# Performance work log

Hardware: AMD Instinct MI355X
Metric: run time of the kernel (lower is better)

## Reference

```python
import jax, jax.numpy as jnp
import numpy as np

N = 8192
X_DIM = 256
Y_DIM = 256


def setup_inputs() -> dict:
    key = jax.random.key(0)
    kx, ky, kw = jax.random.split(key, 3)
    x_samples = jax.random.normal(kx, (N, X_DIM), dtype=jnp.float32)
    y_samples = jax.random.normal(ky, (N, Y_DIM), dtype=jnp.float32)
    # kaiming-uniform-ish init for the bilinear weight [x_dim, y_dim]
    bound = float(np.sqrt(6.0 / X_DIM))
    w = jax.random.uniform(kw, (X_DIM, Y_DIM), dtype=jnp.float32,
                           minval=-bound, maxval=bound)
    return {"x_samples": x_samples, "y_samples": y_samples, "w": w}


def reference(x_samples, y_samples, w):
    # Pairwise bilinear scores S[i, b] = x[i] @ W @ y[b]
    # (equivalent to the original's tiled einsum, without O(N^2*dim) tiles)
    n = y_samples.shape[0]
    xw = x_samples @ w                      # [N, y_dim]
    S = xw @ y_samples.T                    # [N, N], S[i, b]
    # T0[i] = S[i, i]; T1.logsumexp(dim=1)[b] = logsumexp_i S[i, b]
    t0_mean = jnp.mean(jnp.diagonal(S))
    lse_mean = jnp.mean(jax.nn.logsumexp(S, axis=0))
    lower_bound = t0_mean - (lse_mean - jnp.log(jnp.float32(n)))
    return lower_bound
```

## Files before the change

### kernel.cpp

```cpp
#include <hip/hip_runtime.h>

typedef __attribute__((ext_vector_type(8))) short bf16x8;
typedef __attribute__((ext_vector_type(4))) float f32x4;
typedef __attribute__((ext_vector_type(8))) int   i32x8;
typedef __attribute__((ext_vector_type(4))) int   i32x4;

union OpU { i32x8 v; i32x4 h[2]; };

__device__ __forceinline__ unsigned short f2bf(float f) {
    unsigned int u = __float_as_uint(f);
    u += 0x7fffu + ((u >> 16) & 1u);
    return (unsigned short)(u >> 16);
}

#define LSE_SHIFT   90.0f
#define LOG2E       1.44269504f
#define SHIFT_L2E   129.842553f

__global__ void cast_w_kernel(const float* __restrict__ w,
                              unsigned short* __restrict__ WT,
                              float* __restrict__ scal)
{
    int idx = blockIdx.x * 256 + threadIdx.x;
    const float4 wv = ((const float4*)w)[idx];
    int k = idx >> 6;
    int n0 = (idx & 63) * 4;
    WT[(size_t)(n0 + 0) * 256 + k] = f2bf(wv.x);
    WT[(size_t)(n0 + 1) * 256 + k] = f2bf(wv.y);
    WT[(size_t)(n0 + 2) * 256 + k] = f2bf(wv.z);
    WT[(size_t)(n0 + 3) * 256 + k] = f2bf(wv.w);
    if (idx == 0) {
        scal[0] = 0.f; scal[1] = 0.f;
        ((unsigned int*)scal)[2] = 0u;
    }
}

__global__ __launch_bounds__(256, 4)
void gemm0_kernel(const float* __restrict__ X, const unsigned short* __restrict__ WT,
                  const float* __restrict__ Y,
                  unsigned char* __restrict__ XWQ, unsigned char* __restrict__ YQ)
{
    __shared__ __align__(16) unsigned short As[64 * 64];
    __shared__ __align__(16) unsigned short Bs[64 * 64];

    const int tid  = threadIdx.x;
    const int lane = tid & 63;
    const int w    = tid >> 6;
    const int wm   = w >> 1, wn = w & 1;
    const int frow = lane & 15, quad = lane >> 4;
    const int rowBase = blockIdx.y * 64;
    const int colBase = blockIdx.x * 64;
    const int lb = blockIdx.y * 4 + blockIdx.x;

#pragma unroll
    for (int it = 0; it < 4; ++it) {
        int idx = lb * 1024 + it * 256 + tid;
        const float4 yv = ((const float4*)Y)[idx];
        int pk = __builtin_amdgcn_cvt_pk_fp8_f32(yv.x, yv.y, 0, 0);
        pk     = __builtin_amdgcn_cvt_pk_fp8_f32(yv.z, yv.w, pk, 1);
        ((int*)YQ)[idx] = pk;
    }

    int aOff[2][2], bOff[2][2];
#pragma unroll
    for (int mi = 0; mi < 2; ++mi)
#pragma unroll
        for (int kk = 0; kk < 2; ++kk) {
            int ka = kk * 4 + quad;
            int ra = wm * 32 + mi * 16 + frow;
            aOff[mi][kk] = ra * 64 + ((ka ^ (ra & 7)) << 3);
            int rb = wn * 32 + mi * 16 + frow;
            bOff[mi][kk] = rb * 64 + ((ka ^ (rb & 7)) << 3);
        }

    f32x4 acc[2][2];
#pragma unroll
    for (int i = 0; i < 2; ++i)
#pragma unroll
        for (int j = 0; j < 2; ++j)
            acc[i][j] = f32x4{0.f, 0.f, 0.f, 0.f};

#pragma unroll
    for (int kt = 0; kt < 4; ++kt) {
        const int k0 = kt * 64;
#pragma unroll
        for (int it = 0; it < 2; ++it) {
            int p  = it * 256 + tid;
            int r  = p >> 3;
            int s  = p & 7;
            int kc = s ^ (r & 7);
            const unsigned short* gb = WT + (size_t)(colBase + r) * 256 + k0 + (kc << 3);
            __builtin_amdgcn_global_load_lds(
                (const __attribute__((address_space(1))) void*)gb,
                (__attribute__((address_space(3))) void*)&Bs[p << 3], 16, 0, 0);
        }
#pragma unroll
        for (int it = 0; it < 4; ++it) {
            int fidx = it * 256 + tid;
            int r  = fidx >> 4;
            int c4 = fidx & 15;
            float4 v = *(const float4*)&X[(size_t)(rowBase + r) * 256 + k0 + c4 * 4];
            ushort4 u;
            u.x = f2bf(v.x); u.y = f2bf(v.y); u.z = f2bf(v.z); u.w = f2bf(v.w);
            int slot = (c4 >> 1) ^ (r & 7);
            *(ushort4*)&As[r * 64 + (slot << 3) + (c4 & 1) * 4] = u;
        }
        __syncthreads();
#pragma unroll
        for (int kk = 0; kk < 2; ++kk) {
            bf16x8 a[2], b[2];
#pragma unroll
            for (int mi = 0; mi < 2; ++mi) a[mi] = *(const bf16x8*)&As[aOff[mi][kk]];
#pragma unroll
            for (int ni = 0; ni < 2; ++ni) b[ni] = *(const bf16x8*)&Bs[bOff[ni][kk]];
#pragma unroll
            for (int mi = 0; mi < 2; ++mi)
#pragma unroll
                for (int ni = 0; ni < 2; ++ni)
                    acc[mi][ni] = __builtin_amdgcn_mfma_f32_16x16x32_bf16(
                        a[mi], b[ni], acc[mi][ni], 0, 0, 0);
        }
        __syncthreads();
    }

#pragma unroll
    for (int mi = 0; mi < 2; ++mi)
#pragma unroll
        for (int ni = 0; ni < 2; ++ni)
#pragma unroll
            for (int r2 = 0; r2 < 4; ++r2) {
                int row = rowBase + wm * 32 + mi * 16 + quad * 4 + r2;
                int col = colBase + wn * 32 + ni * 16 + frow;
                float v = acc[mi][ni][r2];
                int q = __builtin_amdgcn_cvt_pk_fp8_f32(v, v, 0, 0);
                XWQ[(size_t)row * 256 + col] = (unsigned char)(q & 0xff);
            }
}

__global__ __launch_bounds__(512, 2)
void gemm1_kernel(const unsigned char* __restrict__ A,
                  const unsigned char* __restrict__ B,
                  float* __restrict__ P, float* __restrict__ scal)
{
    __shared__ __align__(16) unsigned char As[2 * 256 * 128];
    __shared__ __align__(16) unsigned char Bs[2 * 256 * 128];
    __shared__ float lsebuf[1024];

    const int tid  = threadIdx.x;
    const int lane = tid & 63;
    const int w    = tid >> 6;
    const int wm   = w >> 1;
    const int wn   = w & 1;
    const int frow = lane & 15, quad = lane >> 4;

    const int bid = blockIdx.y * 32 + blockIdx.x;
    const int swz = (bid & 7) * 128 + (bid >> 3);
    const int by  = swz >> 5, bx = swz & 31;
    const int rowBase = by * 256, colBase = bx * 256;

    const unsigned char* gaP[4];
    const unsigned char* gbP[4];
    unsigned int ldsP[4];
#pragma unroll
    for (int it = 0; it < 4; ++it) {
        int p  = it * 512 + tid;
        int r  = p >> 3;
        int s  = p & 7;
        int kc = s ^ (r & 7);
        gaP[it] = A + (size_t)(rowBase + r) * 256 + (kc << 4);
        gbP[it] = B + (size_t)(colBase + r) * 256 + (kc << 4);
        ldsP[it] = p << 4;
    }

    const int c0 = quad * 2;
    int aAdr[4][2], bAdr[8][2];
#pragma unroll
    for (int mi = 0; mi < 4; ++mi) {
        int ra = wm * 64 + mi * 16 + frow;
        aAdr[mi][0] = ra * 128 + (((c0    ) ^ (ra & 7)) << 4);
        aAdr[mi][1] = ra * 128 + (((c0 + 1) ^ (ra & 7)) << 4);
    }
#pragma unroll
    for (int ni = 0; ni < 8; ++ni) {
        int rb = wn * 128 + ni * 16 + frow;
        bAdr[ni][0] = rb * 128 + (((c0    ) ^ (rb & 7)) << 4);
        bAdr[ni][1] = rb * 128 + (((c0 + 1) ^ (rb & 7)) << 4);
    }

    f32x4 acc[4][8];
#pragma unroll
    for (int i = 0; i < 4; ++i)
#pragma unroll
        for (int j = 0; j < 8; ++j)
            acc[i][j] = f32x4{0.f, 0.f, 0.f, 0.f};

#define STAGE(GOFF, LOFF)                                                     \
    _Pragma("unroll")                                                         \
    for (int it = 0; it < 4; ++it) {                                          \
        __builtin_amdgcn_global_load_lds(                                     \
            (const __attribute__((address_space(1))) void*)(gaP[it] + (GOFF)),\
            (__attribute__((address_space(3))) void*)&As[ldsP[it] + (LOFF)],  \
            16, 0, 0);                                                        \
        __builtin_amdgcn_global_load_lds(                                     \
            (const __attribute__((address_space(1))) void*)(gbP[it] + (GOFF)),\
            (__attribute__((address_space(3))) void*)&Bs[ldsP[it] + (LOFF)],  \
            16, 0, 0);                                                        \
    }

#define COMPUTE(LOFF)                                                         \
    {                                                                         \
        i32x8 a[4];                                                           \
        _Pragma("unroll")                                                     \
        for (int mi = 0; mi < 4; ++mi) {                                      \
            OpU u;                                                            \
            u.h[0] = *(const i32x4*)&As[aAdr[mi][0] + (LOFF)];                \
            u.h[1] = *(const i32x4*)&As[aAdr[mi][1] + (LOFF)];                \
            a[mi] = u.v;                                                      \
        }                                                                     \
        _Pragma("unroll")                                                     \
        for (int ni = 0; ni < 8; ++ni) {                                      \
            OpU ub;                                                           \
            ub.h[0] = *(const i32x4*)&Bs[bAdr[ni][0] + (LOFF)];               \
            ub.h[1] = *(const i32x4*)&Bs[bAdr[ni][1] + (LOFF)];               \
            i32x8 b = ub.v;                                                   \
            _Pragma("unroll")                                                 \
            for (int mi = 0; mi < 4; ++mi)                                    \
                acc[mi][ni] = __builtin_amdgcn_mfma_scale_f32_16x16x128_f8f6f4(\
                    a[mi], b, acc[mi][ni], 0, 0, 0, 0x7f7f7f7f, 0, 0x7f7f7f7f);\
        }                                                                     \
    }

    STAGE(0, 0);
    __syncthreads();
    STAGE(128, 32768);
    COMPUTE(0);
    __syncthreads();
    COMPUTE(32768);

#pragma unroll
    for (int ni = 0; ni < 8; ++ni) {
        float ssum = 0.f;
#pragma unroll
        for (int mi = 0; mi < 4; ++mi)
#pragma unroll
            for (int r2 = 0; r2 < 4; ++r2)
                ssum += __builtin_amdgcn_exp2f(
                    __fmaf_rn(acc[mi][ni][r2], LOG2E, -SHIFT_L2E));
        ssum += __shfl_xor(ssum, 16);
        ssum += __shfl_xor(ssum, 32);
        if (quad == 0)
            lsebuf[wm * 256 + wn * 128 + ni * 16 + frow] = ssum;
    }
    if (bx == by && (wm >> 1) == wn) {
        float v = 0.f;
#pragma unroll
        for (int mi = 0; mi < 4; ++mi)
#pragma unroll
            for (int ni = 0; ni < 8; ++ni)
                if (wm * 4 + mi == wn * 8 + ni) {
#pragma unroll
                    for (int r2 = 0; r2 < 4; ++r2)
                        if (quad * 4 + r2 == frow) v += acc[mi][ni][r2];
                }
#pragma unroll
        for (int o = 1; o < 64; o <<= 1) v += __shfl_xor(v, o);
        if (lane == 0) atomicAdd(&scal[0], v);
    }
    __syncthreads();
    if (tid < 256) {
        P[(size_t)by * 8192 + colBase + tid]
            = lsebuf[tid] + lsebuf[256 + tid] + lsebuf[512 + tid] + lsebuf[768 + tid];
    }
#undef STAGE
#undef COMPUTE
}

__global__ void combine_kernel(const float* __restrict__ P, float* __restrict__ scal,
                               float* __restrict__ out)
{
    __shared__ float red[256];
    const int tid = threadIdx.x;
    const int col = blockIdx.x * 256 + tid;
    float s = 0.f;
#pragma unroll 16
    for (int j = 0; j < 32; ++j)
        s += P[(size_t)j * 8192 + col];
    red[tid] = LSE_SHIFT + logf(s);
    __syncthreads();
#pragma unroll
    for (int o = 128; o > 0; o >>= 1) {
        if (tid < o) red[tid] += red[tid + o];
        __syncthreads();
    }
    if (tid == 0) {
        atomicAdd(&scal[1], red[0]);
        __threadfence();
        unsigned int old = __hip_atomic_fetch_add((unsigned int*)&scal[2], 1u,
                                                  __ATOMIC_ACQ_REL, __HIP_MEMORY_SCOPE_AGENT);
        if (old == 31u) {
            float t0 = __hip_atomic_load(&scal[0], __ATOMIC_RELAXED, __HIP_MEMORY_SCOPE_AGENT);
            float ls = __hip_atomic_load(&scal[1], __ATOMIC_RELAXED, __HIP_MEMORY_SCOPE_AGENT);
            const float invN = 1.f / 8192.f;
            out[0] = t0 * invN - (ls * invN - logf(8192.f));
        }
    }
}

extern "C" void kernel_launch(void* const* d_in, const int* in_sizes, int n_in,
                              void* d_out, int out_size, void* d_ws, size_t ws_size,
                              hipStream_t stream)
{
    const float* x = (const float*)d_in[0];
    const float* y = (const float*)d_in[1];
    const float* w = (const float*)d_in[2];
    float* out = (float*)d_out;

    char* ws = (char*)d_ws;
    unsigned char*  YQ  = (unsigned char*)(ws);
    unsigned char*  XWQ = (unsigned char*)(ws + 0x200000);
    unsigned short* WT  = (unsigned short*)(ws + 0x400000);
    float*          P   = (float*)        (ws + 0x420000);
    float*          scal= (float*)        (ws + 0x620000);

    cast_w_kernel<<<64, 256, 0, stream>>>(w, WT, scal);
    gemm0_kernel<<<dim3(4, 128), 256, 0, stream>>>(x, WT, y, XWQ, YQ);
    gemm1_kernel<<<dim3(32, 32), 512, 0, stream>>>(XWQ, YQ, P, scal);
    combine_kernel<<<32, 256, 0, stream>>>(P, scal, out);
}
```

Baseline: 108.0 us.

## Fuse gemm0, gemm1 and combine into one cooperative persistent kernel

Replaces three kernel launches with a single cooperative kernel of 256 blocks that runs the XW GEMM, then the pairwise fp8 GEMM with the logsumexp epilogue, then the final reduction, separated by grid-wide syncs. In the second phase each block keeps a 256-column Y tile resident in LDS and loops over four row tiles, prefetching the next A tile, so B is reused instead of being reloaded. This is meant to remove launch gaps and tail effects between stages. It adds grid.sync overhead and a fixed grid of 256 blocks at 2 blocks per CU occupancy, which limits parallelism in the first phase and requires every block to be co-resident.

```diff
diff --git a/kernel.cpp b/kernel.cpp
--- a/kernel.cpp
+++ b/kernel.cpp
@@ -1,4 +1,7 @@
 #include <hip/hip_runtime.h>
+#include <hip/hip_cooperative_groups.h>
+
+namespace cg = cooperative_groups;
 
 typedef __attribute__((ext_vector_type(8))) short bf16x8;
 typedef __attribute__((ext_vector_type(4))) float f32x4;
@@ -35,193 +38,194 @@
     }
 }
 
-__global__ __launch_bounds__(256, 4)
-void gemm0_kernel(const float* __restrict__ X, const unsigned short* __restrict__ WT,
+__global__ __launch_bounds__(512, 2)
+void fused_kernel(const float* __restrict__ X,
+                  const unsigned short* __restrict__ WT,
                   const float* __restrict__ Y,
-                  unsigned char* __restrict__ XWQ, unsigned char* __restrict__ YQ)
+                  unsigned char* __restrict__ XWQ,
+                  unsigned char* __restrict__ YQ,
+                  float* __restrict__ P,
+                  float* __restrict__ scal,
+                  float* __restrict__ out)
 {
-    __shared__ __align__(16) unsigned short As[64 * 64];
-    __shared__ __align__(16) unsigned short Bs[64 * 64];
-
-    const int tid  = threadIdx.x;
-    const int lane = tid & 63;
-    const int w    = tid >> 6;
-    const int wm   = w >> 1, wn = w & 1;
-    const int frow = lane & 15, quad = lane >> 4;
-    const int rowBase = blockIdx.y * 64;
-    const int colBase = blockIdx.x * 64;
-    const int lb = blockIdx.y * 4 + blockIdx.x;
+    __shared__ __align__(16) unsigned char AsB[65536];
+    __shared__ __align__(16) unsigned char BsB[65536];
+    __shared__ float lsebuf[1024];
+
+    cg::grid_group grid = cg::this_grid();
+
+    const int tid = threadIdx.x;
+    const int bid = blockIdx.x;
 
 #pragma unroll
     for (int it = 0; it < 4; ++it) {
-        int idx = lb * 1024 + it * 256 + tid;
+        int idx = bid * 2048 + it * 512 + tid;
         const float4 yv = ((const float4*)Y)[idx];
         int pk = __builtin_amdgcn_cvt_pk_fp8_f32(yv.x, yv.y, 0, 0);
         pk     = __builtin_amdgcn_cvt_pk_fp8_f32(yv.z, yv.w, pk, 1);
         ((int*)YQ)[idx] = pk;
     }
-
-    int aOff[2][2], bOff[2][2];
-#pragma unroll
-    for (int mi = 0; mi < 2; ++mi)
-#pragma unroll
-        for (int kk = 0; kk < 2; ++kk) {
-            int ka = kk * 4 + quad;
-            int ra = wm * 32 + mi * 16 + frow;
-            aOff[mi][kk] = ra * 64 + ((ka ^ (ra & 7)) << 3);
-            int rb = wn * 32 + mi * 16 + frow;
-            bOff[mi][kk] = rb * 64 + ((ka ^ (rb & 7)) << 3);
-        }
-
-    f32x4 acc[2][2];
-#pragma unroll
-    for (int i = 0; i < 2; ++i)
-#pragma unroll
-        for (int j = 0; j < 2; ++j)
-            acc[i][j] = f32x4{0.f, 0.f, 0.f, 0.f};
-
-#pragma unroll
-    for (int kt = 0; kt < 4; ++kt) {
-        const int k0 = kt * 64;
-#pragma unroll
-        for (int it = 0; it < 2; ++it) {
-            int p  = it * 256 + tid;
-            int r  = p >> 3;
+    {
+        const int sub  = tid >> 8;
+        const int stid = tid & 255;
+        const int sl   = stid & 63;
+        const int sw   = stid >> 6;
+        const int wm   = sw >> 1, wn = sw & 1;
+        const int frow = sl & 15, quad = sl >> 4;
+        const int rowBase = (bid >> 1) * 64;
+        const int colBase = ((bid & 1) * 2 + sub) * 64;
+        unsigned short* As0 = (unsigned short*)(AsB + sub * 16384);
+        unsigned short* Bs0 = (unsigned short*)(BsB + sub * 16384);
+
+        int aOff[2][2], bOff[2][2];
+#pragma unroll
+        for (int mi = 0; mi < 2; ++mi)
+#pragma unroll
+            for (int kk = 0; kk < 2; ++kk) {
+                int ka = kk * 4 + quad;
+                int ra = wm * 32 + mi * 16 + frow;
+                aOff[mi][kk] = ra * 64 + ((ka ^ (ra & 7)) << 3);
+                int rb = wn * 32 + mi * 16 + frow;
+                bOff[mi][kk] = rb * 64 + ((ka ^ (rb & 7)) << 3);
+            }
+
+        f32x4 acc[2][2];
+#pragma unroll
+        for (int i = 0; i < 2; ++i)
+#pragma unroll
+            for (int j = 0; j < 2; ++j)
+                acc[i][j] = f32x4{0.f, 0.f, 0.f, 0.f};
+
+#pragma unroll
+        for (int kt = 0; kt < 4; ++kt) {
+            const int k0 = kt * 64;
+#pragma unroll
+            for (int it = 0; it < 2; ++it) {
+                int p  = it * 256 + stid;
+                int r  = p >> 3;
+                int s  = p & 7;
+                int kc = s ^ (r & 7);
+                const unsigned short* gb = WT + (size_t)(colBase + r) * 256 + k0 + (kc << 3);
+                __builtin_amdgcn_global_load_lds(
+                    (const __attribute__((address_space(1))) void*)gb,
+                    (__attribute__((address_space(3))) void*)&Bs0[p << 3], 16, 0, 0);
+            }
+#pragma unroll
+            for (int it = 0; it < 4; ++it) {
+                int fidx = it * 256 + stid;
+                int r  = fidx >> 4;
+                int c4 = fidx & 15;
+                float4 v = *(const float4*)&X[(size_t)(rowBase + r) * 256 + k0 + c4 * 4];
+                ushort4 u;
+                u.x = f2bf(v.x); u.y = f2bf(v.y); u.z = f2bf(v.z); u.w = f2bf(v.w);
+                int slot = (c4 >> 1) ^ (r & 7);
+                *(ushort4*)&As0[r * 64 + (slot << 3) + (c4 & 1) * 4] = u;
+            }
+            __syncthreads();
+#pragma unroll
+            for (int kk = 0; kk < 2; ++kk) {
+                bf16x8 a[2], b[2];
+#pragma unroll
+                for (int mi = 0; mi < 2; ++mi) a[mi] = *(const bf16x8*)&As0[aOff[mi][kk]];
+#pragma unroll
+                for (int ni = 0; ni < 2; ++ni) b[ni] = *(const bf16x8*)&Bs0[bOff[ni][kk]];
+#pragma unroll
+                for (int mi = 0; mi < 2; ++mi)
+#pragma unroll
+                    for (int ni = 0; ni < 2; ++ni)
+                        acc[mi][ni] = __builtin_amdgcn_mfma_f32_16x16x32_bf16(
+                            a[mi], b[ni], acc[mi][ni], 0, 0, 0);
+            }
+            __syncthreads();
+        }
+
+#pragma unroll
+        for (int mi = 0; mi < 2; ++mi)
+#pragma unroll
+            for (int ni = 0; ni < 2; ++ni)
+#pragma unroll
+                for (int r2 = 0; r2 < 4; ++r2) {
+                    int row = rowBase + wm * 32 + mi * 16 + quad * 4 + r2;
+                    int col = colBase + wn * 32 + ni * 16 + frow;
+                    float v = acc[mi][ni][r2];
+                    int q = __builtin_amdgcn_cvt_pk_fp8_f32(v, v, 0, 0);
+                    XWQ[(size_t)row * 256 + col] = (unsigned char)(q & 0xff);
+                }
+    }
+    __threadfence();
+    grid.sync();
+    __threadfence();
+
+    {
+        const int lane = tid & 63;
+        const int w    = tid >> 6;
+        const int wm   = w >> 1, wn = w & 1;
+        const int frow = lane & 15, quad = lane >> 4;
+        const int xcd  = bid & 7;
+        const int bx   = bid >> 3;
+        const int colBase = bx * 256;
+        const int by0  = xcd * 4;
+
+        int off0[4];
+        unsigned int ldsP[4];
+#pragma unroll
+        for (int it = 0; it < 4; ++it) {
+            int p  = it * 512 + tid;
+            int rr = p >> 3;
             int s  = p & 7;
-            int kc = s ^ (r & 7);
-            const unsigned short* gb = WT + (size_t)(colBase + r) * 256 + k0 + (kc << 3);
-            __builtin_amdgcn_global_load_lds(
-                (const __attribute__((address_space(1))) void*)gb,
-                (__attribute__((address_space(3))) void*)&Bs[p << 3], 16, 0, 0);
-        }
-#pragma unroll
-        for (int it = 0; it < 4; ++it) {
-            int fidx = it * 256 + tid;
-            int r  = fidx >> 4;
-            int c4 = fidx & 15;
-            float4 v = *(const float4*)&X[(size_t)(rowBase + r) * 256 + k0 + c4 * 4];
-            ushort4 u;
-            u.x = f2bf(v.x); u.y = f2bf(v.y); u.z = f2bf(v.z); u.w = f2bf(v.w);
-            int slot = (c4 >> 1) ^ (r & 7);
-            *(ushort4*)&As[r * 64 + (slot << 3) + (c4 & 1) * 4] = u;
-        }
-        __syncthreads();
-#pragma unroll
-        for (int kk = 0; kk < 2; ++kk) {
-            bf16x8 a[2], b[2];
-#pragma unroll
-            for (int mi = 0; mi < 2; ++mi) a[mi] = *(const bf16x8*)&As[aOff[mi][kk]];
-#pragma unroll
-            for (int ni = 0; ni < 2; ++ni) b[ni] = *(const bf16x8*)&Bs[bOff[ni][kk]];
-#pragma unroll
-            for (int mi = 0; mi < 2; ++mi)
-#pragma unroll
-                for (int ni = 0; ni < 2; ++ni)
-                    acc[mi][ni] = __builtin_amdgcn_mfma_f32_16x16x32_bf16(
-                        a[mi], b[ni], acc[mi][ni], 0, 0, 0);
-        }
-        __syncthreads();
-    }
-
-#pragma unroll
-    for (int mi = 0; mi < 2; ++mi)
-#pragma unroll
-        for (int ni = 0; ni < 2; ++ni)
-#pragma unroll
-            for (int r2 = 0; r2 < 4; ++r2) {
-                int row = rowBase + wm * 32 + mi * 16 + quad * 4 + r2;
-                int col = colBase + wn * 32 + ni * 16 + frow;
-                float v = acc[mi][ni][r2];
-                int q = __builtin_amdgcn_cvt_pk_fp8_f32(v, v, 0, 0);
-                XWQ[(size_t)row * 256 + col] = (unsigned char)(q & 0xff);
-            }
-}
-
-__global__ __launch_bounds__(512, 2)
-void gemm1_kernel(const unsigned char* __restrict__ A,
-                  const unsigned char* __restrict__ B,
-                  float* __restrict__ P, float* __restrict__ scal)
-{
-    __shared__ __align__(16) unsigned char As[2 * 256 * 128];
-    __shared__ __align__(16) unsigned char Bs[2 * 256 * 128];
-    __shared__ float lsebuf[1024];
-
-    const int tid  = threadIdx.x;
-    const int lane = tid & 63;
-    const int w    = tid >> 6;
-    const int wm   = w >> 1;
-    const int wn   = w & 1;
-    const int frow = lane & 15, quad = lane >> 4;
-
-    const int bid = blockIdx.y * 32 + blockIdx.x;
-    const int swz = (bid & 7) * 128 + (bid >> 3);
-    const int by  = swz >> 5, bx = swz & 31;
-    const int rowBase = by * 256, colBase = bx * 256;
-
-    const unsigned char* gaP[4];
-    const unsigned char* gbP[4];
-    unsigned int ldsP[4];
-#pragma unroll
-    for (int it = 0; it < 4; ++it) {
-        int p  = it * 512 + tid;
-        int r  = p >> 3;
-        int s  = p & 7;
-        int kc = s ^ (r & 7);
-        gaP[it] = A + (size_t)(rowBase + r) * 256 + (kc << 4);
-        gbP[it] = B + (size_t)(colBase + r) * 256 + (kc << 4);
-        ldsP[it] = p << 4;
-    }
-
-    const int c0 = quad * 2;
-    int aAdr[4][2], bAdr[8][2];
-#pragma unroll
-    for (int mi = 0; mi < 4; ++mi) {
-        int ra = wm * 64 + mi * 16 + frow;
-        aAdr[mi][0] = ra * 128 + (((c0    ) ^ (ra & 7)) << 4);
-        aAdr[mi][1] = ra * 128 + (((c0 + 1) ^ (ra & 7)) << 4);
-    }
-#pragma unroll
-    for (int ni = 0; ni < 8; ++ni) {
-        int rb = wn * 128 + ni * 16 + frow;
-        bAdr[ni][0] = rb * 128 + (((c0    ) ^ (rb & 7)) << 4);
-        bAdr[ni][1] = rb * 128 + (((c0 + 1) ^ (rb & 7)) << 4);
-    }
-
-    f32x4 acc[4][8];
-#pragma unroll
-    for (int i = 0; i < 4; ++i)
-#pragma unroll
-        for (int j = 0; j < 8; ++j)
-            acc[i][j] = f32x4{0.f, 0.f, 0.f, 0.f};
-
-#define STAGE(GOFF, LOFF)                                                     \
+            int kc = s ^ (rr & 7);
+            off0[it] = rr * 256 + (kc << 4);
+            ldsP[it] = p << 4;
+        }
+
+        const int c0 = quad * 2;
+        int aAdr[4][2], bAdr[8][2];
+#pragma unroll
+        for (int mi = 0; mi < 4; ++mi) {
+            int ra = wm * 64 + mi * 16 + frow;
+            aAdr[mi][0] = ra * 128 + (((c0    ) ^ (ra & 7)) << 4);
+            aAdr[mi][1] = ra * 128 + (((c0 + 1) ^ (ra & 7)) << 4);
+        }
+#pragma unroll
+        for (int ni = 0; ni < 8; ++ni) {
+            int rb = wn * 128 + ni * 16 + frow;
+            bAdr[ni][0] = rb * 128 + (((c0    ) ^ (rb & 7)) << 4);
+            bAdr[ni][1] = rb * 128 + (((c0 + 1) ^ (rb & 7)) << 4);
+        }
+
+#define STAGE_A(ROWS, GOFF, LOFF)                                             \
     _Pragma("unroll")                                                         \
-    for (int it = 0; it < 4; ++it) {                                          \
+    for (int it = 0; it < 4; ++it)                                            \
         __builtin_amdgcn_global_load_lds(                                     \
-            (const __attribute__((address_space(1))) void*)(gaP[it] + (GOFF)),\
-            (__attribute__((address_space(3))) void*)&As[ldsP[it] + (LOFF)],  \
-            16, 0, 0);                                                        \
+            (const __attribute__((address_space(1))) void*)                   \
+                (XWQ + (size_t)(ROWS) * 256 + off0[it] + (GOFF)),             \
+            (__attribute__((address_space(3))) void*)&AsB[ldsP[it] + (LOFF)], \
+            16, 0, 0);
+
+#define STAGE_Bp(GOFF, LOFF)                                                  \
+    _Pragma("unroll")                                                         \
+    for (int it = 0; it < 4; ++it)                                            \
         __builtin_amdgcn_global_load_lds(                                     \
-            (const __attribute__((address_space(1))) void*)(gbP[it] + (GOFF)),\
-            (__attribute__((address_space(3))) void*)&Bs[ldsP[it] + (LOFF)],  \
-            16, 0, 0);                                                        \
-    }
-
-#define COMPUTE(LOFF)                                                         \
+            (const __attribute__((address_space(1))) void*)                   \
+                (YQ + (size_t)colBase * 256 + off0[it] + (GOFF)),             \
+            (__attribute__((address_space(3))) void*)&BsB[ldsP[it] + (LOFF)], \
+            16, 0, 0);
+
+#define COMPUTEK(LOFF)                                                        \
     {                                                                         \
         i32x8 a[4];                                                           \
         _Pragma("unroll")                                                     \
         for (int mi = 0; mi < 4; ++mi) {                                      \
             OpU u;                                                            \
-            u.h[0] = *(const i32x4*)&As[aAdr[mi][0] + (LOFF)];                \
-            u.h[1] = *(const i32x4*)&As[aAdr[mi][1] + (LOFF)];                \
+            u.h[0] = *(const i32x4*)&AsB[aAdr[mi][0] + (LOFF)];               \
+            u.h[1] = *(const i32x4*)&AsB[aAdr[mi][1] + (LOFF)];               \
             a[mi] = u.v;                                                      \
         }                                                                     \
         _Pragma("unroll")                                                     \
         for (int ni = 0; ni < 8; ++ni) {                                      \
             OpU ub;                                                           \
-            ub.h[0] = *(const i32x4*)&Bs[bAdr[ni][0] + (LOFF)];               \
-            ub.h[1] = *(const i32x4*)&Bs[bAdr[ni][1] + (LOFF)];               \
+            ub.h[0] = *(const i32x4*)&BsB[bAdr[ni][0] + (LOFF)];              \
+            ub.h[1] = *(const i32x4*)&BsB[bAdr[ni][1] + (LOFF)];              \
             i32x8 b = ub.v;                                                   \
             _Pragma("unroll")                                                 \
             for (int mi = 0; mi < 4; ++mi)                                    \
@@ -230,78 +234,97 @@
         }                                                                     \
     }
 
-    STAGE(0, 0);
-    __syncthreads();
-    STAGE(128, 32768);
-    COMPUTE(0);
-    __syncthreads();
-    COMPUTE(32768);
-
-#pragma unroll
-    for (int ni = 0; ni < 8; ++ni) {
-        float ssum = 0.f;
-#pragma unroll
-        for (int mi = 0; mi < 4; ++mi)
-#pragma unroll
-            for (int r2 = 0; r2 < 4; ++r2)
-                ssum += __builtin_amdgcn_exp2f(
-                    __fmaf_rn(acc[mi][ni][r2], LOG2E, -SHIFT_L2E));
-        ssum += __shfl_xor(ssum, 16);
-        ssum += __shfl_xor(ssum, 32);
-        if (quad == 0)
-            lsebuf[wm * 256 + wn * 128 + ni * 16 + frow] = ssum;
-    }
-    if (bx == by && (wm >> 1) == wn) {
-        float v = 0.f;
-#pragma unroll
-        for (int mi = 0; mi < 4; ++mi)
-#pragma unroll
-            for (int ni = 0; ni < 8; ++ni)
-                if (wm * 4 + mi == wn * 8 + ni) {
+        STAGE_Bp(0, 0);
+        STAGE_Bp(128, 32768);
+        STAGE_A(by0 * 256, 0, 0);
+        __syncthreads();
+
+        for (int r = 0; r < 4; ++r) {
+            const int by = by0 + r;
+            const int rowBase = by * 256;
+
+            f32x4 acc[4][8];
+#pragma unroll
+            for (int i = 0; i < 4; ++i)
+#pragma unroll
+                for (int j = 0; j < 8; ++j)
+                    acc[i][j] = f32x4{0.f, 0.f, 0.f, 0.f};
+
+            STAGE_A(rowBase, 128, 32768);
+            COMPUTEK(0);
+            __syncthreads();
+            if (r < 3) STAGE_A(rowBase + 256, 0, 0);
+            COMPUTEK(32768);
+
+#pragma unroll
+            for (int ni = 0; ni < 8; ++ni) {
+                float ssum = 0.f;
+#pragma unroll
+                for (int mi = 0; mi < 4; ++mi)
 #pragma unroll
                     for (int r2 = 0; r2 < 4; ++r2)
-                        if (quad * 4 + r2 == frow) v += acc[mi][ni][r2];
-                }
-#pragma unroll
-        for (int o = 1; o < 64; o <<= 1) v += __shfl_xor(v, o);
-        if (lane == 0) atomicAdd(&scal[0], v);
-    }
-    __syncthreads();
-    if (tid < 256) {
-        P[(size_t)by * 8192 + colBase + tid]
-            = lsebuf[tid] + lsebuf[256 + tid] + lsebuf[512 + tid] + lsebuf[768 + tid];
-    }
-#undef STAGE
-#undef COMPUTE
-}
-
-__global__ void combine_kernel(const float* __restrict__ P, float* __restrict__ scal,
-                               float* __restrict__ out)
-{
-    __shared__ float red[256];
-    const int tid = threadIdx.x;
-    const int col = blockIdx.x * 256 + tid;
-    float s = 0.f;
-#pragma unroll 16
-    for (int j = 0; j < 32; ++j)
-        s += P[(size_t)j * 8192 + col];
-    red[tid] = LSE_SHIFT + logf(s);
-    __syncthreads();
-#pragma unroll
-    for (int o = 128; o > 0; o >>= 1) {
-        if (tid < o) red[tid] += red[tid + o];
+                        ssum += __builtin_amdgcn_exp2f(
+                            __fmaf_rn(acc[mi][ni][r2], LOG2E, -SHIFT_L2E));
+                ssum += __shfl_xor(ssum, 16);
+                ssum += __shfl_xor(ssum, 32);
+                if (quad == 0)
+                    lsebuf[wm * 256 + wn * 128 + ni * 16 + frow] = ssum;
+            }
+            if (bx == by && (wm >> 1) == wn) {
+                float v = 0.f;
+#pragma unroll
+                for (int mi = 0; mi < 4; ++mi)
+#pragma unroll
+                    for (int ni = 0; ni < 8; ++ni)
+                        if (wm * 4 + mi == wn * 8 + ni) {
+#pragma unroll
+                            for (int r2 = 0; r2 < 4; ++r2)
+                                if (quad * 4 + r2 == frow) v += acc[mi][ni][r2];
+                        }
+#pragma unroll
+                for (int o = 1; o < 64; o <<= 1) v += __shfl_xor(v, o);
+                if (lane == 0) atomicAdd(&scal[0], v);
+            }
+            __syncthreads();
+            if (tid < 256)
+                P[(size_t)by * 8192 + colBase + tid]
+                    = lsebuf[tid] + lsebuf[256 + tid]
+                    + lsebuf[512 + tid] + lsebuf[768 + tid];
+        }
+#undef STAGE_A
+#undef STAGE_Bp
+#undef COMPUTEK
+    }
+    __threadfence();
+    grid.sync();
+    __threadfence();
+
+    if (bid < 32) {
+        if (tid < 256) {
+            const int col = bid * 256 + tid;
+            float s = 0.f;
+#pragma unroll 8
+            for (int j = 0; j < 32; ++j)
+                s += P[(size_t)j * 8192 + col];
+            lsebuf[tid] = LSE_SHIFT + logf(s);
+        }
         __syncthreads();
-    }
-    if (tid == 0) {
-        atomicAdd(&scal[1], red[0]);
-        __threadfence();
-        unsigned int old = __hip_atomic_fetch_add((unsigned int*)&scal[2], 1u,
-                                                  __ATOMIC_ACQ_REL, __HIP_MEMORY_SCOPE_AGENT);
-        if (old == 31u) {
-            float t0 = __hip_atomic_load(&scal[0], __ATOMIC_RELAXED, __HIP_MEMORY_SCOPE_AGENT);
-            float ls = __hip_atomic_load(&scal[1], __ATOMIC_RELAXED, __HIP_MEMORY_SCOPE_AGENT);
-            const float invN = 1.f / 8192.f;
-            out[0] = t0 * invN - (ls * invN - logf(8192.f));
+#pragma unroll
+        for (int o = 128; o > 0; o >>= 1) {
+            if (tid < o) lsebuf[tid] += lsebuf[tid + o];
+            __syncthreads();
+        }
+        if (tid == 0) {
+            atomicAdd(&scal[1], lsebuf[0]);
+            __threadfence();
+            unsigned int old = __hip_atomic_fetch_add((unsigned int*)&scal[2], 1u,
+                                                      __ATOMIC_ACQ_REL, __HIP_MEMORY_SCOPE_AGENT);
+            if (old == 31u) {
+                float t0 = __hip_atomic_load(&scal[0], __ATOMIC_RELAXED, __HIP_MEMORY_SCOPE_AGENT);
+                float ls = __hip_atomic_load(&scal[1], __ATOMIC_RELAXED, __HIP_MEMORY_SCOPE_AGENT);
+                const float invN = 1.f / 8192.f;
+                out[0] = t0 * invN - (ls * invN - logf(8192.f));
+            }
         }
     }
 }
@@ -323,7 +346,9 @@
     float*          scal= (float*)        (ws + 0x620000);
 
     cast_w_kernel<<<64, 256, 0, stream>>>(w, WT, scal);
-    gemm0_kernel<<<dim3(4, 128), 256, 0, stream>>>(x, WT, y, XWQ, YQ);
-    gemm1_kernel<<<dim3(32, 32), 512, 0, stream>>>(XWQ, YQ, P, scal);
-    combine_kernel<<<32, 256, 0, stream>>>(P, scal, out);
+
+    void* args[] = { (void*)&x, (void*)&WT, (void*)&y, (void*)&XWQ,
+                     (void*)&YQ, (void*)&P, (void*)&scal, (void*)&out };
+    hipLaunchCooperativeKernel((const void*)fused_kernel, dim3(256), dim3(512),
+                               args, 0, stream);
 }
```

Result: slower. 332.3 us (+207.8%).
